# Optimization experiments

Hardware: AMD Instinct MI355X
Metric: run time of the kernel (lower is better)

## Reference

```python
import jax, jax.numpy as jnp
import numpy as np

N = 20000
E = 320000
IN_F = 128
HEADS = 8
OUT_F = 32
NEG_SLOPE = 0.2


def setup_inputs() -> dict:
    key = jax.random.key(0)
    k = jax.random.split(key, 8)
    x = jax.random.normal(k[0], (N, IN_F), dtype=jnp.float32)
    edge_index = jax.random.randint(k[1], (2, E), 0, N, dtype=jnp.int32)
    # Linear weights stored torch-style: [out, in]
    scale = 1.0 / np.sqrt(IN_F)
    W = jax.random.normal(k[2], (HEADS * OUT_F, IN_F), dtype=jnp.float32) * scale
    W1 = jax.random.normal(k[3], (HEADS * OUT_F, IN_F), dtype=jnp.float32) * scale
    W2 = jax.random.normal(k[4], (HEADS * OUT_F, IN_F), dtype=jnp.float32) * scale
    att = jax.random.normal(k[5], (1, HEADS, OUT_F), dtype=jnp.float32) * 0.1
    bias = jnp.zeros((HEADS * OUT_F,), dtype=jnp.float32)
    return {"x": x, "edge_index": edge_index, "W": W, "W1": W1, "W2": W2,
            "att": att, "bias": bias}


def reference(x, edge_index, W, W1, W2, att, bias):
    n, heads, out_f = x.shape[0], att.shape[1], att.shape[2]
    src, dst = edge_index[0], edge_index[1]

    # Node projections: [N, H, F]
    h_src = (x @ W1.T).reshape(n, heads, out_f)
    h_dst = (x @ W2.T).reshape(n, heads, out_f)
    values = (x @ W.T).reshape(n, heads, out_f)

    # Edge-wise GATv2 logits: a^T LeakyReLU(W1 h_i + W2 h_j)  -> [E, H]
    att_input = jax.nn.leaky_relu(h_src[src] + h_dst[dst], negative_slope=NEG_SLOPE)
    logits = jnp.einsum('ehf,hf->eh', att_input, att[0])

    # Segment softmax over incoming edges of each dst node (stable).
    seg_max = jax.ops.segment_max(logits, dst, num_segments=n)  # [N, H]
    exp_l = jnp.exp(logits - seg_max[dst])
    denom = jax.ops.segment_sum(exp_l, dst, num_segments=n)     # [N, H]
    weights = exp_l / denom[dst]                                # [E, H]

    # Weighted aggregation of source values into dst nodes.
    weighted = weights[:, :, None] * values[src]                # [E, H, F]
    out = jax.ops.segment_sum(weighted, dst, num_segments=n)    # [N, H, F]

    out = out.reshape(n, heads * out_f) + bias
    return out
```

## Files before the change

### kernel.cpp

```cpp
#include <hip/hip_runtime.h>
#include <math.h>

#define NN 20000
#define EE 320000
#define KF 128
#define HO 256
#define CAP 96

typedef __attribute__((ext_vector_type(8))) short short8;
typedef __attribute__((ext_vector_type(4))) float f32x4;
typedef __attribute__((ext_vector_type(2))) _Float16 half2_t;

static __device__ __forceinline__ unsigned short f2bf(float f) {
    union { float f; unsigned u; } v; v.f = f;
    unsigned u = v.u;
    u += 0x7fffu + ((u >> 16) & 1u);
    return (unsigned short)(u >> 16);
}
static __device__ __forceinline__ unsigned short f2h(float f) {
    _Float16 h = (_Float16)f;
    return __builtin_bit_cast(unsigned short, h);
}
static __device__ __forceinline__ float dot2f(half2_t a, half2_t b, float c) {
#if __has_builtin(__builtin_amdgcn_fdot2)
    return __builtin_amdgcn_fdot2(a, b, c, false);
#else
    return c + (float)a[0] * (float)b[0] + (float)a[1] * (float)b[1];
#endif
}

__global__ __launch_bounds__(256) void prep_kernel(
    const float* __restrict__ x, const float* __restrict__ W0,
    const float* __restrict__ W1, const float* __restrict__ W2,
    unsigned short* __restrict__ xb, unsigned short* __restrict__ wb,
    int* __restrict__ cursor)
{
    const int b = blockIdx.x;
    const int t = threadIdx.x;
    if (b < 96) {
        const int m = b >> 5;
        const float* __restrict__ Wm = (m == 0) ? W0 : (m == 1) ? W1 : W2;
        int idx = (b & 31) * 1024 + t * 4;
        float4 v = *(const float4*)(Wm + idx);
        ushort4 o;
        o.x = f2bf(v.x); o.y = f2bf(v.y); o.z = f2bf(v.z); o.w = f2bf(v.w);
        *(ushort4*)(wb + (size_t)m * 32768 + idx) = o;
    } else if (b < 2596) {
        size_t i = (size_t)(b - 96) * 1024 + t * 4;
        float4 v = *(const float4*)(x + i);
        ushort4 o;
        o.x = f2bf(v.x); o.y = f2bf(v.y); o.z = f2bf(v.z); o.w = f2bf(v.w);
        *(ushort4*)(xb + i) = o;
    } else {
        int i = (b - 2596) * 256 + t;
        if (i < NN) cursor[i] = 0;
    }
}

__global__ __launch_bounds__(256, 4) void mid_kernel(
    const unsigned short* __restrict__ xb, const unsigned short* __restrict__ wb,
    unsigned short* __restrict__ hv, unsigned short* __restrict__ hdst,
    const int* __restrict__ ei, int* __restrict__ cursor, int* __restrict__ csr_src)
{
    const int bid = blockIdx.x;
    if (bid < 1250) {
        const int e = bid * 256 + threadIdx.x;
        if (e < EE) {
            int s = ei[e];
            int d = ei[EE + e];
            int pos = atomicAdd(&cursor[d], 1);
            if (pos < CAP) csr_src[d * CAP + pos] = s;
        }
        return;
    }
    const int pb = bid - 1250;
    const int m  = (pb < 313) ? 0 : (pb < 626) ? 1 : 2;
    const int bx = pb - m * 313;
    const unsigned short* __restrict__ Wm = wb + (size_t)m * 32768;
    unsigned short* __restrict__ dstp = (m == 2) ? hdst : hv;
    const int voff = (m == 0) ? 4 : 0;

    const int w    = threadIdx.x >> 6;
    const int lane = threadIdx.x & 63;
    const int lr   = lane & 15;
    const int q    = lane >> 4;
    const int cb   = w * 64;

    short8 Bf[4][4];
#pragma unroll
    for (int nt = 0; nt < 4; ++nt)
#pragma unroll
        for (int ks = 0; ks < 4; ++ks)
            Bf[nt][ks] = *(const short8*)(Wm + (size_t)(cb + nt * 16 + lr) * KF + ks * 32 + q * 8);

    const int rb = bx * 64;

#pragma unroll
    for (int it = 0; it < 4; ++it) {
        const int r0 = rb + it * 16;

        short8 Af[4];
        const int arow = r0 + lr;
#pragma unroll
        for (int ks = 0; ks < 4; ++ks) {
            Af[ks] = (short8){0,0,0,0,0,0,0,0};
            if (arow < NN)
                Af[ks] = *(const short8*)(xb + (size_t)arow * KF + ks * 32 + q * 8);
        }

        f32x4 acc[4];
#pragma unroll
        for (int nt = 0; nt < 4; ++nt) acc[nt] = (f32x4){0.f, 0.f, 0.f, 0.f};

#pragma unroll
        for (int ks = 0; ks < 4; ++ks)
#pragma unroll
            for (int nt = 0; nt < 4; ++nt)
                acc[nt] = __builtin_amdgcn_mfma_f32_16x16x32_bf16(Af[ks], Bf[nt][ks], acc[nt], 0, 0, 0);

#pragma unroll
        for (int nt = 0; nt < 4; ++nt) {
            const int f = cb + nt * 16 + lr;
#pragma unroll
            for (int r = 0; r < 4; ++r) {
                const int row = r0 + q * 4 + r;
                if (row < NN) {
                    const unsigned short hval = f2h(acc[nt][r]);
                    if (m == 2) dstp[(size_t)row * 256 + f] = hval;
                    else        dstp[(size_t)row * 512 + ((f >> 2) << 3) + (f & 3) + voff] = hval;
                }
            }
        }
    }
}

__global__ __launch_bounds__(256) void gat_kernel(
    const unsigned short* __restrict__ hv, const unsigned short* __restrict__ hdst,
    const float* __restrict__ att, const float* __restrict__ bias,
    const int* __restrict__ cursor, const int* __restrict__ csr_src,
    float* __restrict__ out)
{
    const int w    = threadIdx.x >> 6;
    const int d    = blockIdx.x * 4 + w;
    const int lane = threadIdx.x & 63;
    const int col  = lane * 4;

    const float4 av = *(const float4*)(att + col);
    const float LOG2E = 1.4426950408889634f;
    const float s6 = 0.6f * LOG2E, s4 = 0.4f * LOG2E;
    const half2_t a6_01 = { (_Float16)(s6 * av.x), (_Float16)(s6 * av.y) };
    const half2_t a6_23 = { (_Float16)(s6 * av.z), (_Float16)(s6 * av.w) };
    const half2_t a4_01 = { (_Float16)(s4 * av.x), (_Float16)(s4 * av.y) };
    const half2_t a4_23 = { (_Float16)(s4 * av.z), (_Float16)(s4 * av.w) };
    const float4 b4 = *(const float4*)(bias + col);

    const uint2 hdb = *(const uint2*)(hdst + (size_t)d * HO + col);
    const half2_t hd01 = __builtin_bit_cast(half2_t, hdb.x);
    const half2_t hd23 = __builtin_bit_cast(half2_t, hdb.y);

    int deg = cursor[d];
    if (deg > CAP) deg = CAP;

    int sreg = (lane < deg) ? csr_src[d * CAP + lane] : 0;

    float l = 0.f;
    float o0 = 0.f, o1 = 0.f, o2 = 0.f, o3 = 0.f;

#define EDGE_CALC(G, VMUL)                                                    \
    {                                                                         \
        half2_t z01 = __builtin_bit_cast(half2_t, G.x) + hd01;                \
        half2_t z23 = __builtin_bit_cast(half2_t, G.y) + hd23;                \
        unsigned zu01 = __builtin_bit_cast(unsigned, z01) & 0x7FFF7FFFu;      \
        unsigned zu23 = __builtin_bit_cast(unsigned, z23) & 0x7FFF7FFFu;      \
        float p = dot2f(a6_01, z01,                                           \
                  dot2f(a6_23, z23,                                           \
                  dot2f(a4_01, __builtin_bit_cast(half2_t, zu01),             \
                  dot2f(a4_23, __builtin_bit_cast(half2_t, zu23), 0.f))));    \
        p += __shfl_xor(p, 1); p += __shfl_xor(p, 2); p += __shfl_xor(p, 4);  \
        const float e = __builtin_amdgcn_exp2f(p) * (VMUL);                   \
        l += e;                                                               \
        const half2_t v01 = __builtin_bit_cast(half2_t, G.z);                 \
        const half2_t v23 = __builtin_bit_cast(half2_t, G.w);                 \
        o0 = fmaf((float)v01[0], e, o0);                                      \
        o1 = fmaf((float)v01[1], e, o1);                                      \
        o2 = fmaf((float)v23[0], e, o2);                                      \
        o3 = fmaf((float)v23[1], e, o3);                                      \
    }

    const int ng = (deg < 64) ? deg : 64;
    for (int i = 0; i < ng; i += 8) {
        int   jj[8];
        float mm[8];
#pragma unroll
        for (int u = 0; u < 8; ++u) {
            const int j = i + u;
            jj[u] = (j < ng) ? j : (ng - 1);
            mm[u] = (j < ng) ? 1.f : 0.f;
        }
        uint4 G[8];
#pragma unroll
        for (int u = 0; u < 8; ++u) {
            const int s = __shfl(sreg, jj[u]);
            G[u] = *(const uint4*)(hv + (size_t)s * 512 + lane * 8);
        }
#pragma unroll
        for (int u = 0; u < 8; ++u) EDGE_CALC(G[u], mm[u]);
    }
    for (int j = 64; j < deg; ++j) {
        const int s0 = csr_src[d * CAP + j];
        const uint4 g = *(const uint4*)(hv + (size_t)s0 * 512 + lane * 8);
        EDGE_CALC(g, 1.f);
    }
#undef EDGE_CALC

    const float inv = (deg > 0) ? 1.f / l : 0.f;
    float4 res;
    res.x = fmaf(o0, inv, b4.x);
    res.y = fmaf(o1, inv, b4.y);
    res.z = fmaf(o2, inv, b4.z);
    res.w = fmaf(o3, inv, b4.w);
    *(float4*)(out + (size_t)d * HO + col) = res;
}

extern "C" void kernel_launch(void* const* d_in, const int* in_sizes, int n_in,
                              void* d_out, int out_size, void* d_ws, size_t ws_size,
                              hipStream_t stream) {
    const float* x    = (const float*)d_in[0];
    const int*   ei   = (const int*)d_in[1];
    const float* W0   = (const float*)d_in[2];
    const float* W1   = (const float*)d_in[3];
    const float* W2   = (const float*)d_in[4];
    const float* att  = (const float*)d_in[5];
    const float* bias = (const float*)d_in[6];
    float* out = (float*)d_out;

    char* p = (char*)d_ws;
    unsigned short* hv   = (unsigned short*)p; p += (size_t)NN * 512 * 2;
    unsigned short* hdst = (unsigned short*)p; p += (size_t)NN * HO * 2;
    unsigned short* xb   = (unsigned short*)p; p += (size_t)NN * KF * 2;
    unsigned short* wb   = (unsigned short*)p; p += (size_t)3 * 32768 * 2;
    int* cursor  = (int*)p; p += (size_t)NN * sizeof(int);
    int* csr_src = (int*)p; p += (size_t)NN * CAP * sizeof(int);

    prep_kernel<<<2675, 256, 0, stream>>>(x, W0, W1, W2, xb, wb, cursor);
    mid_kernel<<<2189, 256, 0, stream>>>(xb, wb, hv, hdst, ei, cursor, csr_src);
    gat_kernel<<<NN / 4, 256, 0, stream>>>(hv, hdst, att, bias, cursor, csr_src, out);
}
```

Baseline: 158.8 us.

## Store source attention projection in custom 8-bit e3m4 and split gather buffers

The source-side attention projection (x@W1) is now stored as a custom 8-bit e3m4 float, and the values projection goes into its own fp16 buffer instead of an interleaved fp16 array. This cuts the per-edge gather from 16 to 12 bytes per lane. The logit computation moves from packed fp16 dot2 to fp32 with an explicit leaky ReLU. Weight conversion to bf16 now happens inside the GEMM kernel instead of in the prep kernel. The cost is that the 8-bit format clamps magnitudes to [1/32, 7.75] with only 4 mantissa bits, which may break accuracy; the gathers also become two separate, smaller loads per edge.

```diff
diff --git a/kernel.cpp b/kernel.cpp
--- a/kernel.cpp
+++ b/kernel.cpp
@@ -21,45 +21,52 @@
     _Float16 h = (_Float16)f;
     return __builtin_bit_cast(unsigned short, h);
 }
-static __device__ __forceinline__ float dot2f(half2_t a, half2_t b, float c) {
-#if __has_builtin(__builtin_amdgcn_fdot2)
-    return __builtin_amdgcn_fdot2(a, b, c, false);
-#else
-    return c + (float)a[0] * (float)b[0] + (float)a[1] * (float)b[1];
-#endif
+
+static __device__ __forceinline__ unsigned f_to_e3m4(float f) {
+    const unsigned uf = __builtin_bit_cast(unsigned, f);
+    float a = fabsf(f);
+    a = fminf(fmaxf(a, 0.03125f), 7.75f);
+    const unsigned ua = __builtin_bit_cast(unsigned, a);
+    unsigned code = (ua - (122u << 23) + (1u << 18)) >> 19;
+    code = (code > 127u) ? 127u : code;
+    return ((uf >> 31) << 7) | code;
+}
+static __device__ __forceinline__ float e3m4_to_f(unsigned b) {
+    return __builtin_bit_cast(float,
+        ((b & 0x80u) << 24) | (((b & 0x7fu) << 19) + (122u << 23)));
+}
+static __device__ __forceinline__ void e3m4x4_to_f(unsigned w, float& f0, float& f1,
+                                                   float& f2, float& f3) {
+    f0 = e3m4_to_f(w & 0xffu);
+    f1 = e3m4_to_f((w >> 8) & 0xffu);
+    f2 = e3m4_to_f((w >> 16) & 0xffu);
+    f3 = e3m4_to_f(w >> 24);
 }
 
 __global__ __launch_bounds__(256) void prep_kernel(
-    const float* __restrict__ x, const float* __restrict__ W0,
-    const float* __restrict__ W1, const float* __restrict__ W2,
-    unsigned short* __restrict__ xb, unsigned short* __restrict__ wb,
+    const float* __restrict__ x, unsigned short* __restrict__ xb,
     int* __restrict__ cursor)
 {
     const int b = blockIdx.x;
     const int t = threadIdx.x;
-    if (b < 96) {
-        const int m = b >> 5;
-        const float* __restrict__ Wm = (m == 0) ? W0 : (m == 1) ? W1 : W2;
-        int idx = (b & 31) * 1024 + t * 4;
-        float4 v = *(const float4*)(Wm + idx);
-        ushort4 o;
-        o.x = f2bf(v.x); o.y = f2bf(v.y); o.z = f2bf(v.z); o.w = f2bf(v.w);
-        *(ushort4*)(wb + (size_t)m * 32768 + idx) = o;
-    } else if (b < 2596) {
-        size_t i = (size_t)(b - 96) * 1024 + t * 4;
+    if (b < 2500) {
+        size_t i = (size_t)b * 1024 + t * 4;
         float4 v = *(const float4*)(x + i);
         ushort4 o;
         o.x = f2bf(v.x); o.y = f2bf(v.y); o.z = f2bf(v.z); o.w = f2bf(v.w);
         *(ushort4*)(xb + i) = o;
     } else {
-        int i = (b - 2596) * 256 + t;
+        int i = (b - 2500) * 256 + t;
         if (i < NN) cursor[i] = 0;
     }
 }
 
 __global__ __launch_bounds__(256, 4) void mid_kernel(
-    const unsigned short* __restrict__ xb, const unsigned short* __restrict__ wb,
-    unsigned short* __restrict__ hv, unsigned short* __restrict__ hdst,
+    const unsigned short* __restrict__ xb,
+    const float* __restrict__ W0, const float* __restrict__ W1,
+    const float* __restrict__ W2,
+    unsigned short* __restrict__ vb, unsigned char* __restrict__ h8,
+    unsigned short* __restrict__ hdst,
     const int* __restrict__ ei, int* __restrict__ cursor, int* __restrict__ csr_src)
 {
     const int bid = blockIdx.x;
@@ -76,9 +83,7 @@
     const int pb = bid - 1250;
     const int m  = (pb < 313) ? 0 : (pb < 626) ? 1 : 2;
     const int bx = pb - m * 313;
-    const unsigned short* __restrict__ Wm = wb + (size_t)m * 32768;
-    unsigned short* __restrict__ dstp = (m == 2) ? hdst : hv;
-    const int voff = (m == 0) ? 4 : 0;
+    const float* __restrict__ Wf = (m == 0) ? W0 : (m == 1) ? W1 : W2;
 
     const int w    = threadIdx.x >> 6;
     const int lane = threadIdx.x & 63;
@@ -88,10 +93,20 @@
 
     short8 Bf[4][4];
 #pragma unroll
-    for (int nt = 0; nt < 4; ++nt)
-#pragma unroll
-        for (int ks = 0; ks < 4; ++ks)
-            Bf[nt][ks] = *(const short8*)(Wm + (size_t)(cb + nt * 16 + lr) * KF + ks * 32 + q * 8);
+    for (int nt = 0; nt < 4; ++nt) {
+        const float* __restrict__ wrow = Wf + (size_t)(cb + nt * 16 + lr) * KF;
+#pragma unroll
+        for (int ks = 0; ks < 4; ++ks) {
+            float4 wa = *(const float4*)(wrow + ks * 32 + q * 8);
+            float4 wc = *(const float4*)(wrow + ks * 32 + q * 8 + 4);
+            short8 bf;
+            bf[0] = (short)f2bf(wa.x); bf[1] = (short)f2bf(wa.y);
+            bf[2] = (short)f2bf(wa.z); bf[3] = (short)f2bf(wa.w);
+            bf[4] = (short)f2bf(wc.x); bf[5] = (short)f2bf(wc.y);
+            bf[6] = (short)f2bf(wc.z); bf[7] = (short)f2bf(wc.w);
+            Bf[nt][ks] = bf;
+        }
+    }
 
     const int rb = bx * 64;
 
@@ -125,9 +140,10 @@
             for (int r = 0; r < 4; ++r) {
                 const int row = r0 + q * 4 + r;
                 if (row < NN) {
-                    const unsigned short hval = f2h(acc[nt][r]);
-                    if (m == 2) dstp[(size_t)row * 256 + f] = hval;
-                    else        dstp[(size_t)row * 512 + ((f >> 2) << 3) + (f & 3) + voff] = hval;
+                    const float val = acc[nt][r];
+                    if (m == 1)      h8[(size_t)row * 256 + f] = (unsigned char)f_to_e3m4(val);
+                    else if (m == 0) vb[(size_t)row * 256 + f] = f2h(val);
+                    else             hdst[(size_t)row * 256 + f] = f2h(val);
                 }
             }
         }
@@ -135,7 +151,8 @@
 }
 
 __global__ __launch_bounds__(256) void gat_kernel(
-    const unsigned short* __restrict__ hv, const unsigned short* __restrict__ hdst,
+    const unsigned short* __restrict__ vb, const unsigned char* __restrict__ h8,
+    const unsigned short* __restrict__ hdst,
     const float* __restrict__ att, const float* __restrict__ bias,
     const int* __restrict__ cursor, const int* __restrict__ csr_src,
     float* __restrict__ out)
@@ -145,18 +162,16 @@
     const int lane = threadIdx.x & 63;
     const int col  = lane * 4;
 
-    const float4 av = *(const float4*)(att + col);
     const float LOG2E = 1.4426950408889634f;
-    const float s6 = 0.6f * LOG2E, s4 = 0.4f * LOG2E;
-    const half2_t a6_01 = { (_Float16)(s6 * av.x), (_Float16)(s6 * av.y) };
-    const half2_t a6_23 = { (_Float16)(s6 * av.z), (_Float16)(s6 * av.w) };
-    const half2_t a4_01 = { (_Float16)(s4 * av.x), (_Float16)(s4 * av.y) };
-    const half2_t a4_23 = { (_Float16)(s4 * av.z), (_Float16)(s4 * av.w) };
+    float4 av = *(const float4*)(att + col);
+    av.x *= LOG2E; av.y *= LOG2E; av.z *= LOG2E; av.w *= LOG2E;
     const float4 b4 = *(const float4*)(bias + col);
 
     const uint2 hdb = *(const uint2*)(hdst + (size_t)d * HO + col);
     const half2_t hd01 = __builtin_bit_cast(half2_t, hdb.x);
     const half2_t hd23 = __builtin_bit_cast(half2_t, hdb.y);
+    const float hd0 = (float)hd01[0], hd1 = (float)hd01[1];
+    const float hd2 = (float)hd23[0], hd3 = (float)hd23[1];
 
     int deg = cursor[d];
     if (deg > CAP) deg = CAP;
@@ -166,21 +181,20 @@
     float l = 0.f;
     float o0 = 0.f, o1 = 0.f, o2 = 0.f, o3 = 0.f;
 
-#define EDGE_CALC(G, VMUL)                                                    \
+#define EDGE_CALC(V, H, VMUL)                                                 \
     {                                                                         \
-        half2_t z01 = __builtin_bit_cast(half2_t, G.x) + hd01;                \
-        half2_t z23 = __builtin_bit_cast(half2_t, G.y) + hd23;                \
-        unsigned zu01 = __builtin_bit_cast(unsigned, z01) & 0x7FFF7FFFu;      \
-        unsigned zu23 = __builtin_bit_cast(unsigned, z23) & 0x7FFF7FFFu;      \
-        float p = dot2f(a6_01, z01,                                           \
-                  dot2f(a6_23, z23,                                           \
-                  dot2f(a4_01, __builtin_bit_cast(half2_t, zu01),             \
-                  dot2f(a4_23, __builtin_bit_cast(half2_t, zu23), 0.f))));    \
+        float s0f, s1f, s2f, s3f;                                             \
+        e3m4x4_to_f(H, s0f, s1f, s2f, s3f);                                   \
+        float z0 = s0f + hd0, z1 = s1f + hd1;                                 \
+        float z2 = s2f + hd2, z3 = s3f + hd3;                                 \
+        z0 = fmaxf(z0, 0.2f * z0); z1 = fmaxf(z1, 0.2f * z1);                 \
+        z2 = fmaxf(z2, 0.2f * z2); z3 = fmaxf(z3, 0.2f * z3);                 \
+        float p = fmaf(av.x, z0, av.y * z1) + fmaf(av.z, z2, av.w * z3);      \
         p += __shfl_xor(p, 1); p += __shfl_xor(p, 2); p += __shfl_xor(p, 4);  \
         const float e = __builtin_amdgcn_exp2f(p) * (VMUL);                   \
         l += e;                                                               \
-        const half2_t v01 = __builtin_bit_cast(half2_t, G.z);                 \
-        const half2_t v23 = __builtin_bit_cast(half2_t, G.w);                 \
+        const half2_t v01 = __builtin_bit_cast(half2_t, V.x);                 \
+        const half2_t v23 = __builtin_bit_cast(half2_t, V.y);                 \
         o0 = fmaf((float)v01[0], e, o0);                                      \
         o1 = fmaf((float)v01[1], e, o1);                                      \
         o2 = fmaf((float)v23[0], e, o2);                                      \
@@ -197,19 +211,22 @@
             jj[u] = (j < ng) ? j : (ng - 1);
             mm[u] = (j < ng) ? 1.f : 0.f;
         }
-        uint4 G[8];
+        uint2 V[8];
+        unsigned H[8];
 #pragma unroll
         for (int u = 0; u < 8; ++u) {
             const int s = __shfl(sreg, jj[u]);
-            G[u] = *(const uint4*)(hv + (size_t)s * 512 + lane * 8);
-        }
-#pragma unroll
-        for (int u = 0; u < 8; ++u) EDGE_CALC(G[u], mm[u]);
+            V[u] = *(const uint2*)(vb + (size_t)s * 256 + col);
+            H[u] = *(const unsigned*)(h8 + (size_t)s * 256 + col);
+        }
+#pragma unroll
+        for (int u = 0; u < 8; ++u) EDGE_CALC(V[u], H[u], mm[u]);
     }
     for (int j = 64; j < deg; ++j) {
         const int s0 = csr_src[d * CAP + j];
-        const uint4 g = *(const uint4*)(hv + (size_t)s0 * 512 + lane * 8);
-        EDGE_CALC(g, 1.f);
+        const uint2 v = *(const uint2*)(vb + (size_t)s0 * 256 + col);
+        const unsigned h = *(const unsigned*)(h8 + (size_t)s0 * 256 + col);
+        EDGE_CALC(v, h, 1.f);
     }
 #undef EDGE_CALC
 
@@ -235,14 +252,14 @@
     float* out = (float*)d_out;
 
     char* p = (char*)d_ws;
-    unsigned short* hv   = (unsigned short*)p; p += (size_t)NN * 512 * 2;
+    unsigned short* vb   = (unsigned short*)p; p += (size_t)NN * HO * 2;
     unsigned short* hdst = (unsigned short*)p; p += (size_t)NN * HO * 2;
+    unsigned char*  h8   = (unsigned char*)p;  p += (size_t)NN * HO;
     unsigned short* xb   = (unsigned short*)p; p += (size_t)NN * KF * 2;
-    unsigned short* wb   = (unsigned short*)p; p += (size_t)3 * 32768 * 2;
     int* cursor  = (int*)p; p += (size_t)NN * sizeof(int);
     int* csr_src = (int*)p; p += (size_t)NN * CAP * sizeof(int);
 
-    prep_kernel<<<2675, 256, 0, stream>>>(x, W0, W1, W2, xb, wb, cursor);
-    mid_kernel<<<2189, 256, 0, stream>>>(xb, wb, hv, hdst, ei, cursor, csr_src);
-    gat_kernel<<<NN / 4, 256, 0, stream>>>(hv, hdst, att, bias, cursor, csr_src, out);
-}
+    prep_kernel<<<2579, 256, 0, stream>>>(x, xb, cursor);
+    mid_kernel<<<2189, 256, 0, stream>>>(xb, W0, W1, W2, vb, h8, hdst, ei, cursor, csr_src);
+    gat_kernel<<<NN / 4, 256, 0, stream>>>(vb, h8, hdst, att, bias, cursor, csr_src, out);
+}
```

Result: slower. 192.7 us (+21.3%).
